# Optimization experiments

Hardware: AMD Instinct MI355X
Metric: run time of the kernel (lower is better)

## Reference

```python
import jax, jax.numpy as jnp
import numpy as np

HEADS = 8
DIM_HEAD = 64


def setup_inputs() -> dict:
    key = jax.random.key(0)
    ks = jax.random.split(key, 8)
    B, L, m = 4, 1024, 64
    Dq, Dc = 512, 256
    inner = HEADS * DIM_HEAD  # 512
    x = jax.random.normal(ks[0], (B, L, Dq), dtype=jnp.float32)
    context = jax.random.normal(ks[1], (B, L, m, Dc), dtype=jnp.float32)
    mask = jax.random.randint(ks[2], (B, L, m), 0, 2).astype(bool)
    # guarantee at least one valid token per (b,l) row
    mask = mask.at[:, :, 0].set(True)
    bias = jax.random.normal(ks[3], (B, L, m), dtype=jnp.float32)
    s = 0.02
    Wq = jax.random.normal(ks[4], (Dq, inner), dtype=jnp.float32) * s
    Wk = jax.random.normal(ks[5], (Dc, inner), dtype=jnp.float32) * s
    Wv = jax.random.normal(ks[6], (Dc, inner), dtype=jnp.float32) * s
    Wo = jax.random.normal(ks[7], (inner, Dq), dtype=jnp.float32) * s
    bo = jnp.zeros((Dq,), dtype=jnp.float32)
    return {"x": x, "context": context, "mask": mask, "bias": bias,
            "Wq": Wq, "Wk": Wk, "Wv": Wv, "Wo": Wo, "bo": bo}


def reference(x, context, mask, bias, Wq, Wk, Wv, Wo, bo):
    B, L, Dq = x.shape
    m = context.shape[2]
    scale = DIM_HEAD ** (-0.5)
    # projections
    Q = (x @ Wq).reshape(B, L, HEADS, DIM_HEAD)                 # b l h d
    K = (context @ Wk).reshape(B, L, m, HEADS, DIM_HEAD)        # b l m h d
    V = (context @ Wv).reshape(B, L, m, HEADS, DIM_HEAD)        # b l m h d
    scores = jnp.einsum('blhd,blmhd->blhm', Q, K) * scale       # b l h m
    scores = scores + bias[:, :, None, :]
    scores = jnp.where(mask[:, :, None, :], scores, -jnp.inf)
    attn = jax.nn.softmax(scores, axis=-1)
    out = jnp.einsum('blhm,blmhd->blhd', attn, V).reshape(B, L, HEADS * DIM_HEAD)
    return out @ Wo + bo
```

## Files before the change

kernel.cpp:

```cpp
#include <hip/hip_runtime.h>
#include <cstddef>


typedef __attribute__((ext_vector_type(8))) short short8;
typedef __attribute__((ext_vector_type(4))) float float4v;

__device__ __forceinline__ short f2bf(float f) {
  unsigned u = __float_as_uint(f);
  return (short)((u + 0x7fffu + ((u >> 16) & 1u)) >> 16);
}

__global__ __launch_bounds__(256) void k_cvt(const float* __restrict__ x,
                                             const float* __restrict__ Wk,
                                             const float* __restrict__ Wv,
                                             short* __restrict__ xb,
                                             short* __restrict__ Wkb,
                                             short* __restrict__ Wvb) {
  size_t i4 = ((size_t)blockIdx.x * 256 + threadIdx.x) * 4;
  const float* src; short* dst; size_t off;
  if (i4 < 2097152)       { src = x;  dst = xb;  off = i4; }
  else if (i4 < 2228224)  { src = Wk; dst = Wkb; off = i4 - 2097152; }
  else                    { src = Wv; dst = Wvb; off = i4 - 2228224; }
  float4 v = *(const float4*)(src + off);
  short4 o; o.x = f2bf(v.x); o.y = f2bf(v.y); o.z = f2bf(v.z); o.w = f2bf(v.w);
  *(short4*)(dst + off) = o;
}

__global__ __launch_bounds__(256) void k_tcvt(const float* __restrict__ in,
                                              short* __restrict__ out) {
  int id = blockIdx.x * 256 + threadIdx.x;
  int k = id >> 9, n = id & 511;
  out[(size_t)n * 512 + k] = f2bf(in[(size_t)k * 512 + n]);
}

__global__ __launch_bounds__(256) void k_mm(const short* __restrict__ A,
                                            const short* __restrict__ Bt,
                                            const float* __restrict__ bias,
                                            void* __restrict__ C,
                                            int lda, int ldb, int ldc, int K,
                                            int bShift, int bMask, int bHS, int crossAK,
                                            float scale, int storeBF16) {
  __shared__ short As[128 * 72];
  __shared__ short Bs[128 * 72];
  int t = threadIdx.x;
  int n0 = blockIdx.x * 128, m0 = blockIdx.y * 128;
  int hb = n0 >> bShift;
  const short* aBase = A + (size_t)m0 * lda + (size_t)hb * crossAK;
  const short* bBase = Bt + (size_t)(n0 & bMask) * ldb + (size_t)hb * bHS;
  int w = t >> 6, l = t & 63;
  int wm = w & 1, wn = w >> 1;
  int li = l & 15, kq = l >> 4;
  float4v acc[4][4];
#pragma unroll
  for (int i = 0; i < 4; ++i)
#pragma unroll
    for (int j = 0; j < 4; ++j) acc[i][j] = (float4v){0.f, 0.f, 0.f, 0.f};

  for (int k0 = 0; k0 < K; k0 += 64) {
    __syncthreads();
#pragma unroll
    for (int p = 0; p < 4; ++p) {
      int i = p * 256 + t, row = i >> 3, kq8 = i & 7;
      *(uint4*)&As[row * 72 + kq8 * 8] = *(const uint4*)(aBase + (size_t)row * lda + k0 + kq8 * 8);
      *(uint4*)&Bs[row * 72 + kq8 * 8] = *(const uint4*)(bBase + (size_t)row * ldb + k0 + kq8 * 8);
    }
    __syncthreads();
#pragma unroll
    for (int kk = 0; kk < 2; ++kk) {
      short8 af[4], bfr[4];
#pragma unroll
      for (int i = 0; i < 4; ++i) {
        af[i]  = *(const short8*)&As[(wm * 64 + i * 16 + li) * 72 + kk * 32 + kq * 8];
        bfr[i] = *(const short8*)&Bs[(wn * 64 + i * 16 + li) * 72 + kk * 32 + kq * 8];
      }
#pragma unroll
      for (int mi = 0; mi < 4; ++mi)
#pragma unroll
        for (int ni = 0; ni < 4; ++ni)
          acc[mi][ni] = __builtin_amdgcn_mfma_f32_16x16x32_bf16(af[mi], bfr[ni], acc[mi][ni], 0, 0, 0);
    }
  }
#pragma unroll
  for (int ni = 0; ni < 4; ++ni) {
    int col = n0 + wn * 64 + ni * 16 + li;
    float bv = bias ? bias[col] : 0.f;
#pragma unroll
    for (int mi = 0; mi < 4; ++mi)
#pragma unroll
      for (int r = 0; r < 4; ++r) {
        int row = m0 + wm * 64 + mi * 16 + kq * 4 + r;
        float v = fmaf(acc[mi][ni][r], scale, bv);
        if (storeBF16) ((short*)C)[(size_t)row * ldc + col] = f2bf(v);
        else           ((float*)C)[(size_t)row * ldc + col] = v;
      }
  }
}

__global__ __launch_bounds__(256, 3) void k_attn(const float* __restrict__ ctx,
                                                 const short* __restrict__ Qkb,
                                                 const float* __restrict__ bias,
                                                 const int* __restrict__ mask,
                                                 short* __restrict__ CA) {
  __shared__ __align__(16) short uni[256 * 72];
  __shared__ __align__(16) float S[64][17];
  __shared__ __align__(16) short attn_b[16][72];
  __shared__ float bs[64];
  __shared__ int   msk[64];

  int t = threadIdx.x;
  int r = blockIdx.x;
  int l = t & 63, w = t >> 6;
  int li = l & 15, kq = l >> 4;

  const float* ctxr = ctx + (size_t)r * 16384;
  const short* qrow = Qkb + (size_t)r * 2048;

  uint* az = (uint*)&attn_b[8][0];
  az[t] = 0;
  if (t < 32) az[256 + t] = 0;

  int hq = l & 7;
  short8 qf[8];
#pragma unroll
  for (int ks = 0; ks < 8; ++ks)
    qf[ks] = *(const short8*)(qrow + hq * 256 + ks * 32 + kq * 8);

  if (t < 64) { bs[t] = bias[(size_t)r * 64 + t]; msk[t] = mask[(size_t)r * 64 + t]; }

  short (*mc)[264] = (short (*)[264])uni;
  short (*cm)[72]  = (short (*)[72])uni;

  short4 sv[16];
#pragma unroll
  for (int i = 0; i < 16; ++i) {
    int m = w * 16 + i;
    float4 v = *(const float4*)(ctxr + m * 256 + l * 4);
    short4 b4; b4.x = f2bf(v.x); b4.y = f2bf(v.y); b4.z = f2bf(v.z); b4.w = f2bf(v.w);
    sv[i] = b4;
    *(short4*)&mc[m][l * 4] = b4;
  }
  __syncthreads();

  float4v sacc = (float4v){0.f, 0.f, 0.f, 0.f};
#pragma unroll
  for (int ks = 0; ks < 8; ++ks) {
    short8 af = *(const short8*)&mc[w * 16 + li][ks * 32 + kq * 8];
    sacc = __builtin_amdgcn_mfma_f32_16x16x32_bf16(af, qf[ks], sacc, 0, 0, 0);
  }
#pragma unroll
  for (int rg = 0; rg < 4; ++rg) S[w * 16 + kq * 4 + rg][li] = sacc[rg];
  __syncthreads();

  int m_ = t & 63, h0 = t >> 6;
  bool valid = msk[m_] != 0;
  float b = bs[m_];
  float s0 = valid ? S[m_][h0] + b : -INFINITY;
  float s1 = valid ? S[m_][h0 + 4] + b : -INFINITY;
  float mx0 = s0, mx1 = s1;
#pragma unroll
  for (int o = 32; o > 0; o >>= 1) {
    mx0 = fmaxf(mx0, __shfl_xor(mx0, o, 64));
    mx1 = fmaxf(mx1, __shfl_xor(mx1, o, 64));
  }
  float e0 = __expf(s0 - mx0), e1 = __expf(s1 - mx1);
  float sm0 = e0, sm1 = e1;
#pragma unroll
  for (int o = 32; o > 0; o >>= 1) {
    sm0 += __shfl_xor(sm0, o, 64);
    sm1 += __shfl_xor(sm1, o, 64);
  }
  attn_b[h0][m_]     = f2bf(e0 / sm0);
  attn_b[h0 + 4][m_] = f2bf(e1 / sm1);

#pragma unroll
  for (int p = 0; p < 4; ++p) {
    int c  = l + p * 64;
    int sl = (l >> 2) + p * 16;
#pragma unroll
    for (int k = 0; k < 4; ++k) {
      int wd[4];
#pragma unroll
      for (int j = 0; j < 4; ++j) {
        int2 two = *(int2*)&sv[4 * k + j];
        int wx = __shfl(two.x, sl, 64);
        int wy = __shfl(two.y, sl, 64);
        wd[j] = (l & 2) ? wy : wx;
      }
      short4 o;
      o.x = (l & 1) ? (short)(wd[0] >> 16) : (short)wd[0];
      o.y = (l & 1) ? (short)(wd[1] >> 16) : (short)wd[1];
      o.z = (l & 1) ? (short)(wd[2] >> 16) : (short)wd[2];
      o.w = (l & 1) ? (short)(wd[3] >> 16) : (short)wd[3];
      *(short4*)&cm[c][w * 16 + k * 4] = o;
    }
  }
  __syncthreads();

  short8 bfr[2];
#pragma unroll
  for (int ks = 0; ks < 2; ++ks)
    bfr[ks] = *(const short8*)&attn_b[li][ks * 32 + kq * 8];
  float4v ca[4];
#pragma unroll
  for (int mi = 0; mi < 4; ++mi) ca[mi] = (float4v){0.f, 0.f, 0.f, 0.f};
#pragma unroll
  for (int mi = 0; mi < 4; ++mi)
#pragma unroll
    for (int ks = 0; ks < 2; ++ks) {
      short8 af = *(const short8*)&cm[w * 64 + mi * 16 + li][ks * 32 + kq * 8];
      ca[mi] = __builtin_amdgcn_mfma_f32_16x16x32_bf16(af, bfr[ks], ca[mi], 0, 0, 0);
    }
  short* car = CA + (size_t)r * 2048;
  if (li < 8) {
#pragma unroll
    for (int mi = 0; mi < 4; ++mi)
#pragma unroll
      for (int rg = 0; rg < 4; ++rg)
        car[li * 256 + w * 64 + mi * 16 + kq * 4 + rg] = f2bf(ca[mi][rg]);
  }
}

extern "C" void kernel_launch(void* const* d_in, const int* in_sizes, int n_in,
                              void* d_out, int out_size, void* d_ws, size_t ws_size,
                              hipStream_t stream) {
  const float* x    = (const float*)d_in[0];
  const float* ctx  = (const float*)d_in[1];
  const int*   mask = (const int*)d_in[2];
  const float* bias = (const float*)d_in[3];
  const float* Wq   = (const float*)d_in[4];
  const float* Wk   = (const float*)d_in[5];
  const float* Wv   = (const float*)d_in[6];
  const float* Wo   = (const float*)d_in[7];
  const float* bo   = (const float*)d_in[8];
  float* out = (float*)d_out;

  char* ws = (char*)d_ws;
  short* xb    = (short*)(ws);
  short* Qb    = (short*)(ws + (4u << 20));
  short* Qkb   = (short*)(ws + (8u << 20));
  short* CAb   = (short*)(ws + (24u << 20));
  short* WqTb  = (short*)(ws + (40u << 20));
  short* WoTb  = (short*)(ws + (40u << 20) + (512u << 10));
  short* Wkb   = (short*)(ws + (41u << 20));
  short* Wvb   = (short*)(ws + (41u << 20) + (256u << 10));
  short* WvoTb = (short*)(ws + (42u << 20));

  hipLaunchKernelGGL(k_cvt,  dim3(2304), dim3(256), 0, stream, x, Wk, Wv, xb, Wkb, Wvb);
  hipLaunchKernelGGL(k_tcvt, dim3(1024), dim3(256), 0, stream, Wq, WqTb);
  hipLaunchKernelGGL(k_tcvt, dim3(1024), dim3(256), 0, stream, Wo, WoTb);
  hipLaunchKernelGGL(k_mm, dim3(16, 4), dim3(256), 0, stream,
                     WoTb, Wvb, (const float*)nullptr, WvoTb,
                     512, 512, 2048, 64, 8, 255, 64, 64, 1.0f, 1);
  hipLaunchKernelGGL(k_mm, dim3(4, 32), dim3(256), 0, stream,
                     xb, WqTb, (const float*)nullptr, Qb,
                     512, 512, 512, 512, 31, 0x7fffffff, 0, 0, 1.0f, 1);
  hipLaunchKernelGGL(k_mm, dim3(16, 32), dim3(256), 0, stream,
                     Qb, Wkb, (const float*)nullptr, Qkb,
                     512, 512, 2048, 64, 8, 255, 64, 64, 0.125f, 1);
  hipLaunchKernelGGL(k_attn, dim3(4096), dim3(256), 0, stream, ctx, Qkb, bias, mask, CAb);
  hipLaunchKernelGGL(k_mm, dim3(4, 32), dim3(256), 0, stream,
                     CAb, WvoTb, bo, out,
                     2048, 2048, 512, 2048, 31, 0x7fffffff, 0, 0, 1.0f, 0);
}
```

Measured before the change: 465.0 us.

## Precompute Wq·Wk product, fuse prep kernels, and halve attention head padding

Precomputes the per-head product Wq·Wkᵀ (scaled) as a weight-only GEMM. The Q projection and the Q·Wk step then collapse into a single x·WqkT GEMM with K=512, removing the intermediate Q buffer and one activation-sized GEMM. The three conversion and transpose kernels are merged into one prep kernel that uses an LDS-tiled transpose for Wo. k_mm gains a templated N tile (64 for small or output GEMMs, giving more blocks) and a transposed bf16 store mode. k_attn drops the 16-wide head padding to 8 to cut LDS use, raising the occupancy hint to 4; this means lanes 8–15 read duplicated attention rows.

```diff
diff --git a/kernel.cpp b/kernel.cpp
--- a/kernel.cpp
+++ b/kernel.cpp
@@ -10,51 +10,75 @@
   return (short)((u + 0x7fffu + ((u >> 16) & 1u)) >> 16);
 }
 
-__global__ __launch_bounds__(256) void k_cvt(const float* __restrict__ x,
-                                             const float* __restrict__ Wk,
-                                             const float* __restrict__ Wv,
-                                             short* __restrict__ xb,
-                                             short* __restrict__ Wkb,
-                                             short* __restrict__ Wvb) {
-  size_t i4 = ((size_t)blockIdx.x * 256 + threadIdx.x) * 4;
-  const float* src; short* dst; size_t off;
-  if (i4 < 2097152)       { src = x;  dst = xb;  off = i4; }
-  else if (i4 < 2228224)  { src = Wk; dst = Wkb; off = i4 - 2097152; }
-  else                    { src = Wv; dst = Wvb; off = i4 - 2228224; }
-  float4 v = *(const float4*)(src + off);
-  short4 o; o.x = f2bf(v.x); o.y = f2bf(v.y); o.z = f2bf(v.z); o.w = f2bf(v.w);
-  *(short4*)(dst + off) = o;
-}
-
-__global__ __launch_bounds__(256) void k_tcvt(const float* __restrict__ in,
-                                              short* __restrict__ out) {
-  int id = blockIdx.x * 256 + threadIdx.x;
-  int k = id >> 9, n = id & 511;
-  out[(size_t)n * 512 + k] = f2bf(in[(size_t)k * 512 + n]);
-}
-
+__global__ __launch_bounds__(256) void k_prep(const float* __restrict__ x,
+                                              const float* __restrict__ Wq,
+                                              const float* __restrict__ Wk,
+                                              const float* __restrict__ Wv,
+                                              const float* __restrict__ Wo,
+                                              short* __restrict__ xb,
+                                              short* __restrict__ Wqb,
+                                              short* __restrict__ Wkb,
+                                              short* __restrict__ Wvb,
+                                              short* __restrict__ WoTb) {
+  __shared__ short lt[64][72];
+  int b = blockIdx.x, t = threadIdx.x;
+  if (b < 2560) {
+    size_t i4 = ((size_t)b * 256 + t) * 4;
+    const float* src; short* dst; size_t off;
+    if (i4 < 2097152)      { src = x;  dst = xb;  off = i4; }
+    else if (i4 < 2359296) { src = Wq; dst = Wqb; off = i4 - 2097152; }
+    else if (i4 < 2490368) { src = Wk; dst = Wkb; off = i4 - 2359296; }
+    else                   { src = Wv; dst = Wvb; off = i4 - 2490368; }
+    float4 v = *(const float4*)(src + off);
+    short4 o; o.x = f2bf(v.x); o.y = f2bf(v.y); o.z = f2bf(v.z); o.w = f2bf(v.w);
+    *(short4*)(dst + off) = o;
+    return;
+  }
+  int tile = b - 2560;
+  int k0 = (tile >> 3) * 64, n0 = (tile & 7) * 64;
+  int rr = t >> 4, cc = t & 15;
+#pragma unroll
+  for (int p = 0; p < 4; ++p) {
+    int k = p * 16 + rr;
+    float4 v = *(const float4*)(Wo + (size_t)(k0 + k) * 512 + n0 + cc * 4);
+    short4 o; o.x = f2bf(v.x); o.y = f2bf(v.y); o.z = f2bf(v.z); o.w = f2bf(v.w);
+    *(short4*)&lt[k][cc * 4] = o;
+  }
+  __syncthreads();
+#pragma unroll
+  for (int p = 0; p < 4; ++p) {
+    int n = p * 16 + rr;
+    short4 o;
+    o.x = lt[cc * 4 + 0][n]; o.y = lt[cc * 4 + 1][n];
+    o.z = lt[cc * 4 + 2][n]; o.w = lt[cc * 4 + 3][n];
+    *(short4*)&WoTb[(size_t)(n0 + n) * 512 + k0 + cc * 4] = o;
+  }
+}
+
+template<int BN>
 __global__ __launch_bounds__(256) void k_mm(const short* __restrict__ A,
                                             const short* __restrict__ Bt,
                                             const float* __restrict__ bias,
                                             void* __restrict__ C,
                                             int lda, int ldb, int ldc, int K,
                                             int bShift, int bMask, int bHS, int crossAK,
-                                            float scale, int storeBF16) {
+                                            float scale, int storeMode) {
   __shared__ short As[128 * 72];
-  __shared__ short Bs[128 * 72];
+  __shared__ short Bs[BN * 72];
   int t = threadIdx.x;
-  int n0 = blockIdx.x * 128, m0 = blockIdx.y * 128;
+  int n0 = blockIdx.x * BN, m0 = blockIdx.y * 128;
   int hb = n0 >> bShift;
   const short* aBase = A + (size_t)m0 * lda + (size_t)hb * crossAK;
   const short* bBase = Bt + (size_t)(n0 & bMask) * ldb + (size_t)hb * bHS;
   int w = t >> 6, l = t & 63;
   int wm = w & 1, wn = w >> 1;
   int li = l & 15, kq = l >> 4;
-  float4v acc[4][4];
+  constexpr int NI = BN / 32;
+  float4v acc[4][NI];
 #pragma unroll
   for (int i = 0; i < 4; ++i)
 #pragma unroll
-    for (int j = 0; j < 4; ++j) acc[i][j] = (float4v){0.f, 0.f, 0.f, 0.f};
+    for (int j = 0; j < NI; ++j) acc[i][j] = (float4v){0.f, 0.f, 0.f, 0.f};
 
   for (int k0 = 0; k0 < K; k0 += 64) {
     __syncthreads();
@@ -62,48 +86,66 @@
     for (int p = 0; p < 4; ++p) {
       int i = p * 256 + t, row = i >> 3, kq8 = i & 7;
       *(uint4*)&As[row * 72 + kq8 * 8] = *(const uint4*)(aBase + (size_t)row * lda + k0 + kq8 * 8);
+    }
+#pragma unroll
+    for (int p = 0; p < BN / 32; ++p) {
+      int i = p * 256 + t, row = i >> 3, kq8 = i & 7;
       *(uint4*)&Bs[row * 72 + kq8 * 8] = *(const uint4*)(bBase + (size_t)row * ldb + k0 + kq8 * 8);
     }
     __syncthreads();
 #pragma unroll
     for (int kk = 0; kk < 2; ++kk) {
-      short8 af[4], bfr[4];
-#pragma unroll
-      for (int i = 0; i < 4; ++i) {
+      short8 af[4], bfr[NI];
+#pragma unroll
+      for (int i = 0; i < 4; ++i)
         af[i]  = *(const short8*)&As[(wm * 64 + i * 16 + li) * 72 + kk * 32 + kq * 8];
-        bfr[i] = *(const short8*)&Bs[(wn * 64 + i * 16 + li) * 72 + kk * 32 + kq * 8];
+#pragma unroll
+      for (int i = 0; i < NI; ++i)
+        bfr[i] = *(const short8*)&Bs[(wn * (BN / 2) + i * 16 + li) * 72 + kk * 32 + kq * 8];
+#pragma unroll
+      for (int mi = 0; mi < 4; ++mi)
+#pragma unroll
+        for (int ni = 0; ni < NI; ++ni)
+          acc[mi][ni] = __builtin_amdgcn_mfma_f32_16x16x32_bf16(af[mi], bfr[ni], acc[mi][ni], 0, 0, 0);
+    }
+  }
+#pragma unroll
+  for (int ni = 0; ni < NI; ++ni) {
+    int col = n0 + wn * (BN / 2) + ni * 16 + li;
+    float bv = bias ? bias[col] : 0.f;
+    if (storeMode == 2) {
+      int row0 = m0 + wm * 64 + kq * 4;
+#pragma unroll
+      for (int mi = 0; mi < 4; ++mi) {
+        short4 o;
+        o.x = f2bf(fmaf(acc[mi][ni][0], scale, bv));
+        o.y = f2bf(fmaf(acc[mi][ni][1], scale, bv));
+        o.z = f2bf(fmaf(acc[mi][ni][2], scale, bv));
+        o.w = f2bf(fmaf(acc[mi][ni][3], scale, bv));
+        *(short4*)&((short*)C)[(size_t)col * ldc + row0 + mi * 16] = o;
       }
+    } else {
 #pragma unroll
       for (int mi = 0; mi < 4; ++mi)
 #pragma unroll
-        for (int ni = 0; ni < 4; ++ni)
-          acc[mi][ni] = __builtin_amdgcn_mfma_f32_16x16x32_bf16(af[mi], bfr[ni], acc[mi][ni], 0, 0, 0);
-    }
-  }
-#pragma unroll
-  for (int ni = 0; ni < 4; ++ni) {
-    int col = n0 + wn * 64 + ni * 16 + li;
-    float bv = bias ? bias[col] : 0.f;
-#pragma unroll
-    for (int mi = 0; mi < 4; ++mi)
-#pragma unroll
-      for (int r = 0; r < 4; ++r) {
-        int row = m0 + wm * 64 + mi * 16 + kq * 4 + r;
-        float v = fmaf(acc[mi][ni][r], scale, bv);
-        if (storeBF16) ((short*)C)[(size_t)row * ldc + col] = f2bf(v);
-        else           ((float*)C)[(size_t)row * ldc + col] = v;
-      }
-  }
-}
-
-__global__ __launch_bounds__(256, 3) void k_attn(const float* __restrict__ ctx,
+        for (int r = 0; r < 4; ++r) {
+          int row = m0 + wm * 64 + mi * 16 + kq * 4 + r;
+          float v = fmaf(acc[mi][ni][r], scale, bv);
+          if (storeMode) ((short*)C)[(size_t)row * ldc + col] = f2bf(v);
+          else           ((float*)C)[(size_t)row * ldc + col] = v;
+        }
+    }
+  }
+}
+
+__global__ __launch_bounds__(256, 4) void k_attn(const float* __restrict__ ctx,
                                                  const short* __restrict__ Qkb,
                                                  const float* __restrict__ bias,
                                                  const int* __restrict__ mask,
                                                  short* __restrict__ CA) {
   __shared__ __align__(16) short uni[256 * 72];
-  __shared__ __align__(16) float S[64][17];
-  __shared__ __align__(16) short attn_b[16][72];
+  __shared__ __align__(16) float S[64][9];
+  __shared__ __align__(16) short attn_b[8][72];
   __shared__ float bs[64];
   __shared__ int   msk[64];
 
@@ -114,10 +156,6 @@
 
   const float* ctxr = ctx + (size_t)r * 16384;
   const short* qrow = Qkb + (size_t)r * 2048;
-
-  uint* az = (uint*)&attn_b[8][0];
-  az[t] = 0;
-  if (t < 32) az[256 + t] = 0;
 
   int hq = l & 7;
   short8 qf[8];
@@ -147,8 +185,10 @@
     short8 af = *(const short8*)&mc[w * 16 + li][ks * 32 + kq * 8];
     sacc = __builtin_amdgcn_mfma_f32_16x16x32_bf16(af, qf[ks], sacc, 0, 0, 0);
   }
-#pragma unroll
-  for (int rg = 0; rg < 4; ++rg) S[w * 16 + kq * 4 + rg][li] = sacc[rg];
+  if (li < 8) {
+#pragma unroll
+    for (int rg = 0; rg < 4; ++rg) S[w * 16 + kq * 4 + rg][li] = sacc[rg];
+  }
   __syncthreads();
 
   int m_ = t & 63, h0 = t >> 6;
@@ -199,7 +239,7 @@
   short8 bfr[2];
 #pragma unroll
   for (int ks = 0; ks < 2; ++ks)
-    bfr[ks] = *(const short8*)&attn_b[li][ks * 32 + kq * 8];
+    bfr[ks] = *(const short8*)&attn_b[li & 7][ks * 32 + kq * 8];
   float4v ca[4];
 #pragma unroll
   for (int mi = 0; mi < 4; ++mi) ca[mi] = (float4v){0.f, 0.f, 0.f, 0.f};
@@ -236,29 +276,23 @@
 
   char* ws = (char*)d_ws;
   short* xb    = (short*)(ws);
-  short* Qb    = (short*)(ws + (4u << 20));
-  short* Qkb   = (short*)(ws + (8u << 20));
-  short* CAb   = (short*)(ws + (24u << 20));
-  short* WqTb  = (short*)(ws + (40u << 20));
-  short* WoTb  = (short*)(ws + (40u << 20) + (512u << 10));
-  short* Wkb   = (short*)(ws + (41u << 20));
-  short* Wvb   = (short*)(ws + (41u << 20) + (256u << 10));
-  short* WvoTb = (short*)(ws + (42u << 20));
-
-  hipLaunchKernelGGL(k_cvt,  dim3(2304), dim3(256), 0, stream, x, Wk, Wv, xb, Wkb, Wvb);
-  hipLaunchKernelGGL(k_tcvt, dim3(1024), dim3(256), 0, stream, Wq, WqTb);
-  hipLaunchKernelGGL(k_tcvt, dim3(1024), dim3(256), 0, stream, Wo, WoTb);
-  hipLaunchKernelGGL(k_mm, dim3(16, 4), dim3(256), 0, stream,
-                     WoTb, Wvb, (const float*)nullptr, WvoTb,
-                     512, 512, 2048, 64, 8, 255, 64, 64, 1.0f, 1);
-  hipLaunchKernelGGL(k_mm, dim3(4, 32), dim3(256), 0, stream,
-                     xb, WqTb, (const float*)nullptr, Qb,
-                     512, 512, 512, 512, 31, 0x7fffffff, 0, 0, 1.0f, 1);
-  hipLaunchKernelGGL(k_mm, dim3(16, 32), dim3(256), 0, stream,
-                     Qb, Wkb, (const float*)nullptr, Qkb,
-                     512, 512, 2048, 64, 8, 255, 64, 64, 0.125f, 1);
-  hipLaunchKernelGGL(k_attn, dim3(4096), dim3(256), 0, stream, ctx, Qkb, bias, mask, CAb);
-  hipLaunchKernelGGL(k_mm, dim3(4, 32), dim3(256), 0, stream,
-                     CAb, WvoTb, bo, out,
-                     2048, 2048, 512, 2048, 31, 0x7fffffff, 0, 0, 1.0f, 0);
-}
+  short* Qkb   = (short*)(ws + (4u << 20));
+  short* CAb   = (short*)(ws + (20u << 20));
+  short* WoTb  = (short*)(ws + (36u << 20));
+  short* Wqb   = (short*)(ws + (36u << 20) + (512u << 10));
+  short* Wkb   = (short*)(ws + (37u << 20));
+  short* Wvb   = (short*)(ws + (37u << 20) + (256u << 10));
+  short* WvoTb = (short*)(ws + (38u << 20));
+  short* WqkTb = (short*)(ws + (40u << 20));
+
+  k_prep<<<dim3(2624), dim3(256), 0, stream>>>(x, Wq, Wk, Wv, Wo, xb, Wqb, Wkb, Wvb, WoTb);
+  k_mm<64><<<dim3(32, 4), dim3(256), 0, stream>>>(WoTb, Wvb, (const float*)nullptr, WvoTb,
+                                                  512, 512, 2048, 64, 8, 255, 64, 64, 1.0f, 1);
+  k_mm<64><<<dim3(32, 4), dim3(256), 0, stream>>>(Wqb, Wkb, (const float*)nullptr, WqkTb,
+                                                  512, 512, 512, 64, 8, 255, 64, 64, 0.125f, 2);
+  k_mm<128><<<dim3(16, 32), dim3(256), 0, stream>>>(xb, WqkTb, (const float*)nullptr, Qkb,
+                                                    512, 512, 2048, 512, 31, 0x7fffffff, 0, 0, 1.0f, 1);
+  k_attn<<<dim3(4096), dim3(256), 0, stream>>>(ctx, Qkb, bias, mask, CAb);
+  k_mm<64><<<dim3(8, 32), dim3(256), 0, stream>>>(CAb, WvoTb, bo, out,
+                                                  2048, 2048, 512, 2048, 31, 0x7fffffff, 0, 0, 1.0f, 0);
+}
```

After: 455.2 us. -2.1%, faster.
